# Kernel tuning notes

Hardware: AMD Instinct MI355X
Metric: run time of the kernel (lower is better)

Reference implementation:

```python
import jax, jax.numpy as jnp
import numpy as np

M, K, N, B, C = 16, 16, 16, 2048, 10


def setup_inputs() -> dict:
    key = jax.random.key(0)
    k1, k2 = jax.random.split(key)
    prediction = jax.random.normal(k1, (M, K, N, B, C), dtype=jnp.float32)
    label = jax.random.randint(k2, (B,), 0, C, dtype=jnp.int64)
    return {"prediction": prediction, "label": label}


def reference(prediction, label):
    # nominal accuracy per (m,k,n) slice, fully vectorized:
    # torch.max(pred, dim=1) -> argmax over class dim; compare to label; mean over batch.
    idx = jnp.argmax(prediction, axis=-1)              # [M,K,N,B]
    corrects = (idx == label[None, None, None, :]).astype(jnp.float32)
    accs = jnp.mean(corrects, axis=-1)                 # [M,K,N], == corrects.sum()/label.numel()
    # scalar=True path: torch.mean(accs)
    return jnp.mean(accs)
```

## Files before the change

### kernel.cpp

```cpp
#include <hip/hip_runtime.h>


#define NSLICE (16 * 16 * 16 * 2048)
#define BATCH 2048
#define NCLS 10

__global__ void eval_init(unsigned int* cnt) {
    if (threadIdx.x == 0 && blockIdx.x == 0) *cnt = 0u;
}

__device__ __forceinline__ int argmax10(const float* f) {
    float best = f[0];
    int bi = 0;
#pragma unroll
    for (int j = 1; j < NCLS; ++j) {
        if (f[j] > best) { best = f[j]; bi = j; }
    }
    return bi;
}

__global__ __launch_bounds__(256) void eval_acc(const float4* __restrict__ pred4,
                                                const int* __restrict__ label,
                                                unsigned int* __restrict__ cnt) {
    const unsigned long long p =
        (unsigned long long)blockIdx.x * blockDim.x + threadIdx.x;

    const float4 v0 = pred4[5 * p + 0];
    const float4 v1 = pred4[5 * p + 1];
    const float4 v2 = pred4[5 * p + 2];
    const float4 v3 = pred4[5 * p + 3];
    const float4 v4 = pred4[5 * p + 4];

    float f[20];
    f[0] = v0.x;  f[1] = v0.y;  f[2] = v0.z;  f[3] = v0.w;
    f[4] = v1.x;  f[5] = v1.y;  f[6] = v1.z;  f[7] = v1.w;
    f[8] = v2.x;  f[9] = v2.y;  f[10] = v2.z; f[11] = v2.w;
    f[12] = v3.x; f[13] = v3.y; f[14] = v3.z; f[15] = v3.w;
    f[16] = v4.x; f[17] = v4.y; f[18] = v4.z; f[19] = v4.w;

    const int b0 = (int)((2ull * p) & (BATCH - 1));
    const int lab0 = label[b0];
    const int lab1 = label[b0 + 1];

    int local = (argmax10(f) == lab0) + (argmax10(f + NCLS) == lab1);

#pragma unroll
    for (int off = 32; off > 0; off >>= 1) local += __shfl_down(local, off, 64);

    __shared__ int wsum[4];
    const int wave = threadIdx.x >> 6;
    const int lane = threadIdx.x & 63;
    if (lane == 0) wsum[wave] = local;
    __syncthreads();
    if (threadIdx.x == 0) {
        const int s = wsum[0] + wsum[1] + wsum[2] + wsum[3];
        atomicAdd(cnt, (unsigned int)s);
    }
}

__global__ void eval_fin(const unsigned int* __restrict__ cnt, float* __restrict__ out) {
    if (threadIdx.x == 0 && blockIdx.x == 0) {
        out[0] = (float)(*cnt) * (1.0f / (float)NSLICE);
    }
}

extern "C" void kernel_launch(void* const* d_in, const int* in_sizes, int n_in,
                              void* d_out, int out_size, void* d_ws, size_t ws_size,
                              hipStream_t stream) {
    const float4* pred4 = (const float4*)d_in[0];
    const int* label = (const int*)d_in[1];
    unsigned int* cnt = (unsigned int*)d_ws;
    float* out = (float*)d_out;

    eval_init<<<1, 1, 0, stream>>>(cnt);

    const int threads = 256;
    const int blocks = (NSLICE / 2) / threads;
    eval_acc<<<blocks, threads, 0, stream>>>(pred4, label, cnt);

    eval_fin<<<1, 1, 0, stream>>>(cnt, out);
}
```

Baseline: 522.8 us.

## Stage predictions through LDS for coalesced loads and drop finalize kernel

```diff
diff --git a/kernel.cpp b/kernel.cpp
--- a/kernel.cpp
+++ b/kernel.cpp
@@ -5,62 +5,64 @@
 #define BATCH 2048
 #define NCLS 10
 
-__global__ void eval_init(unsigned int* cnt) {
-    if (threadIdx.x == 0 && blockIdx.x == 0) *cnt = 0u;
-}
-
-__device__ __forceinline__ int argmax10(const float* f) {
-    float best = f[0];
-    int bi = 0;
-#pragma unroll
-    for (int j = 1; j < NCLS; ++j) {
-        if (f[j] > best) { best = f[j]; bi = j; }
-    }
-    return bi;
+__global__ void eval_init(float* out) {
+    if (threadIdx.x == 0 && blockIdx.x == 0) out[0] = 0.0f;
 }
 
 __global__ __launch_bounds__(256) void eval_acc(const float4* __restrict__ pred4,
                                                 const int* __restrict__ label,
-                                                unsigned int* __restrict__ cnt) {
-    const unsigned long long p =
-        (unsigned long long)blockIdx.x * blockDim.x + threadIdx.x;
+                                                float* __restrict__ out) {
+    __shared__ float4 sh[1280];
+    __shared__ int wsum[4];
 
-    const float4 v0 = pred4[5 * p + 0];
-    const float4 v1 = pred4[5 * p + 1];
-    const float4 v2 = pred4[5 * p + 2];
-    const float4 v3 = pred4[5 * p + 3];
-    const float4 v4 = pred4[5 * p + 4];
+    const int w = threadIdx.x >> 6;
+    const int lane = threadIdx.x & 63;
+
+    const size_t blockF4 = (size_t)blockIdx.x * 1280 + (size_t)w * 320;
+    float4* lw = &sh[w * 320];
+
+#pragma unroll
+    for (int i = 0; i < 5; ++i)
+        lw[i * 64 + lane] = pred4[blockF4 + (size_t)i * 64 + lane];
+
+    __syncthreads();
 
     float f[20];
-    f[0] = v0.x;  f[1] = v0.y;  f[2] = v0.z;  f[3] = v0.w;
-    f[4] = v1.x;  f[5] = v1.y;  f[6] = v1.z;  f[7] = v1.w;
-    f[8] = v2.x;  f[9] = v2.y;  f[10] = v2.z; f[11] = v2.w;
-    f[12] = v3.x; f[13] = v3.y; f[14] = v3.z; f[15] = v3.w;
-    f[16] = v4.x; f[17] = v4.y; f[18] = v4.z; f[19] = v4.w;
+#pragma unroll
+    for (int i = 0; i < 5; ++i) {
+        const float4 v = lw[lane * 5 + i];
+        f[i * 4 + 0] = v.x;
+        f[i * 4 + 1] = v.y;
+        f[i * 4 + 2] = v.z;
+        f[i * 4 + 3] = v.w;
+    }
 
-    const int b0 = (int)((2ull * p) & (BATCH - 1));
+    const int pair = blockIdx.x * 256 + w * 64 + lane;
+    const int b0 = (2 * pair) & (BATCH - 1);
     const int lab0 = label[b0];
     const int lab1 = label[b0 + 1];
 
-    int local = (argmax10(f) == lab0) + (argmax10(f + NCLS) == lab1);
+    int bi0 = 0;
+    float m0 = f[0];
+#pragma unroll
+    for (int j = 1; j < NCLS; ++j)
+        if (f[j] > m0) { m0 = f[j]; bi0 = j; }
+    int bi1 = 0;
+    float m1 = f[NCLS];
+#pragma unroll
+    for (int j = 1; j < NCLS; ++j)
+        if (f[NCLS + j] > m1) { m1 = f[NCLS + j]; bi1 = j; }
+
+    int local = (bi0 == lab0) + (bi1 == lab1);
 
 #pragma unroll
     for (int off = 32; off > 0; off >>= 1) local += __shfl_down(local, off, 64);
 
-    __shared__ int wsum[4];
-    const int wave = threadIdx.x >> 6;
-    const int lane = threadIdx.x & 63;
-    if (lane == 0) wsum[wave] = local;
+    if (lane == 0) wsum[w] = local;
     __syncthreads();
     if (threadIdx.x == 0) {
-        const int s = wsum[0] + wsum[1] + wsum[2] + wsum[3];
-        atomicAdd(cnt, (unsigned int)s);
-    }
-}
-
-__global__ void eval_fin(const unsigned int* __restrict__ cnt, float* __restrict__ out) {
-    if (threadIdx.x == 0 && blockIdx.x == 0) {
-        out[0] = (float)(*cnt) * (1.0f / (float)NSLICE);
+        const float s = (float)(wsum[0] + wsum[1] + wsum[2] + wsum[3]);
+        atomicAdd(out, s * (1.0f / (float)NSLICE));
     }
 }
 
@@ -69,14 +71,9 @@
                               hipStream_t stream) {
     const float4* pred4 = (const float4*)d_in[0];
     const int* label = (const int*)d_in[1];
-    unsigned int* cnt = (unsigned int*)d_ws;
     float* out = (float*)d_out;
 
-    eval_init<<<1, 1, 0, stream>>>(cnt);
+    eval_init<<<1, 64, 0, stream>>>(out);
 
-    const int threads = 256;
-    const int blocks = (NSLICE / 2) / threads;
-    eval_acc<<<blocks, threads, 0, stream>>>(pred4, label, cnt);
-
-    eval_fin<<<1, 1, 0, stream>>>(cnt, out);
+    eval_acc<<<16384, 256, 0, stream>>>(pred4, label, out);
 }
```

Result: slower. 547.2 us (+4.7%).
